# Optimization experiments

Hardware: AMD Instinct MI355X
Metric: run time of the kernel (lower is better)

Reference implementation:

```python
import jax, jax.numpy as jnp
import numpy as np

D_MODEL, N_QUERY, N_HEAD = 1024, 2, 8
D_HEAD = D_MODEL // (N_QUERY * N_HEAD)  # 64
KV = D_HEAD * N_HEAD                    # 512


def setup_inputs() -> dict:
    key = jax.random.key(0)
    ks = jax.random.split(key, 6)
    B, S = 2, 2048
    x = jax.random.normal(ks[0], (B, S, D_MODEL), jnp.float32)
    Wq = jax.random.normal(ks[1], (D_MODEL, D_MODEL), jnp.float32) / np.sqrt(D_MODEL)
    Wk = jax.random.normal(ks[2], (D_MODEL, KV), jnp.float32) / np.sqrt(D_MODEL)
    Wv = jax.random.normal(ks[3], (D_MODEL, KV), jnp.float32) / np.sqrt(D_MODEL)
    memory = jax.random.normal(ks[4], (KV, KV), jnp.float32)
    memory_norm = jnp.ones((KV,), jnp.float32)
    memory_weight = jnp.ones((1,), jnp.float32)
    return {"x": x, "Wq": Wq, "Wk": Wk, "Wv": Wv,
            "memory": memory, "memory_norm": memory_norm,
            "memory_weight": memory_weight}


def reference(x, Wq, Wk, Wv, memory, memory_norm, memory_weight):
    B, S, _ = x.shape
    QH = N_QUERY * N_HEAD
    scale = 1.0 / jnp.sqrt(jnp.float32(D_HEAD))

    q = x @ Wq          # (B,S,D_MODEL)
    k = x @ Wk          # (B,S,KV)
    v = x @ Wv          # (B,S,KV)

    # --- Eq. 6: grouped scaled dot-product attention ---
    q4 = q.reshape(B, S, QH, D_HEAD)                    # flat query split
    k4 = jnp.repeat(k.reshape(B, S, N_HEAD, D_HEAD), N_QUERY, axis=2)  # (B,S,QH,D)
    v4 = jnp.repeat(v.reshape(B, S, N_HEAD, D_HEAD), N_QUERY, axis=2)
    scores = jnp.einsum('bsnd,btnd->bnst', q4, k4) * scale  # (B,QH,S,S)
    probs = jax.nn.softmax(scores, axis=-1)
    a_dot = jnp.einsum('bnst,btnd->bsnd', probs, v4)        # (B,S,QH,D)

    # --- Eq. 7: memory read (grouped over n_query, width n_head*d_head) ---
    sigma_q = jax.nn.elu(q.reshape(B, S, N_QUERY, KV))      # (B,S,Q,KV)
    num = sigma_q @ memory                                   # (B,S,Q,KV)
    den = (sigma_q @ memory_norm)[..., None]                 # (B,S,Q,1)
    a_mem = (num / den).reshape(B, S, QH, D_HEAD)

    # --- Eq. 8/9: memory update (delta rule) ---
    sigma_k = jax.nn.elu(k)                                  # (B,S,KV)
    retrieved = (sigma_k @ memory) / (sigma_k @ memory_norm)[..., None]
    new_memory = memory + jnp.einsum('bsk,bsv->kv', sigma_k, v - retrieved)
    new_memory_norm = memory_norm + jnp.sum(sigma_k, axis=(0, 1))

    # --- Eq. 10: sigmoid-gated fusion ---
    w = jax.nn.sigmoid(memory_weight)                        # (1,)
    out = (a_dot * (1.0 - w) + a_mem * w).reshape(B, S, D_MODEL)
    return out, new_memory, new_memory_norm
```

## Files before the change

kernel.cpp:

```cpp
#include <hip/hip_runtime.h>
#include <hip/hip_bf16.h>

#define BB 2
#define SS 2048
#define DM 1024
#define KVD 512
#define NH 8
#define NQ 2
#define QH 16
#define DH 64
#define MROWS 4096

typedef float f32x4 __attribute__((ext_vector_type(4)));
typedef short short8 __attribute__((ext_vector_type(8)));
typedef short short4v __attribute__((ext_vector_type(4)));
typedef unsigned uint2v __attribute__((ext_vector_type(2)));

__device__ __forceinline__ float elu_f(float x) {
    return x > 0.0f ? x : (__expf(x) - 1.0f);
}

__device__ __forceinline__ short f2bf(float f) {
    union { float f; unsigned u; } v; v.f = f;
    unsigned r = v.u + 0x7FFFu + ((v.u >> 16) & 1u);
    return (short)(r >> 16);
}
__device__ __forceinline__ float bf2f(short s) {
    union { unsigned u; float f; } v;
    v.u = ((unsigned)(unsigned short)s) << 16;
    return v.f;
}
__device__ __forceinline__ unsigned cvtpk(float lo, float hi) {
    unsigned u;
    asm("v_cvt_pk_bf16_f32 %0, %1, %2" : "=v"(u) : "v"(lo), "v"(hi));
    return u;
}

__device__ __forceinline__ int swzs(int row, int byteoff) {
    return (row * 128 + (byteoff ^ ((row & 7) << 4))) >> 1;
}

#define GLD16(gp, lp) __builtin_amdgcn_global_load_lds( \
    (const __attribute__((address_space(1))) void*)(gp), \
    (__attribute__((address_space(3))) void*)(lp), 16, 0, 0)

__device__ __forceinline__ void stage_gl(const short* __restrict__ src, int ld,
                                         int row0, int k0, short* L,
                                         int wv, int lane) {
    const int srow = lane >> 3, sslot = lane & 7;
    #pragma unroll
    for (int i = 0; i < 4; i++) {
        int row = wv * 32 + i * 8 + srow;
        int slot = sslot ^ (row & 7);
        GLD16(&src[(size_t)(row0 + row) * ld + k0 + slot * 8],
              &L[(wv * 32 + i * 8) * 64]);
    }
}

__device__ __forceinline__ void mma_tile(const short* __restrict__ Als,
                                         const short* __restrict__ Bls,
                                         int mb, int nb, int qr, int kg,
                                         f32x4 acc[4][4]) {
    #pragma unroll
    for (int kc = 0; kc < 2; kc++) {
        short8 af[4], bg[4];
        #pragma unroll
        for (int mi = 0; mi < 4; mi++)
            af[mi] = *(const short8*)&Als[swzs(mb + mi * 16 + qr, kc * 64 + kg * 16)];
        #pragma unroll
        for (int ni = 0; ni < 4; ni++)
            bg[ni] = *(const short8*)&Bls[swzs(nb + ni * 16 + qr, kc * 64 + kg * 16)];
        #pragma unroll
        for (int mi = 0; mi < 4; mi++)
            #pragma unroll
            for (int ni = 0; ni < 4; ni++)
                acc[mi][ni] = __builtin_amdgcn_mfma_f32_16x16x32_bf16(
                    af[mi], bg[ni], acc[mi][ni], 0, 0, 0);
    }
}

__global__ __launch_bounds__(256) void convert_x(
        const float* __restrict__ x, short* __restrict__ xb) {
    int i = (blockIdx.x * 256 + threadIdx.x) * 8;
    float4 a = *(const float4*)&x[i];
    float4 b = *(const float4*)&x[i + 4];
    short8 s;
    s[0] = f2bf(a.x); s[1] = f2bf(a.y); s[2] = f2bf(a.z); s[3] = f2bf(a.w);
    s[4] = f2bf(b.x); s[5] = f2bf(b.y); s[6] = f2bf(b.z); s[7] = f2bf(b.w);
    *(short8*)&xb[i] = s;
}

__global__ __launch_bounds__(256) void transpose_w(
        const float* __restrict__ Wq, const float* __restrict__ Wk,
        const float* __restrict__ Wv, short* __restrict__ wtb) {
    __shared__ float Ts[64][65];
    const int k0 = blockIdx.x * 64, n0 = blockIdx.y * 64;
    const float* W; int ld, c0;
    if (n0 < 1024)      { W = Wq; ld = 1024; c0 = n0; }
    else if (n0 < 1536) { W = Wk; ld = 512;  c0 = n0 - 1024; }
    else                { W = Wv; ld = 512;  c0 = n0 - 1536; }
    const int tid = threadIdx.x;
    #pragma unroll
    for (int i = 0; i < 16; i++) {
        int e = tid + 256 * i;
        int kk = e >> 6, nn = e & 63;
        Ts[nn][kk] = W[(size_t)(k0 + kk) * ld + c0 + nn];
    }
    __syncthreads();
    #pragma unroll
    for (int i = 0; i < 16; i++) {
        int e = tid + 256 * i;
        int nn = e >> 6, kk = e & 63;
        wtb[(size_t)(n0 + nn) * 1024 + k0 + kk] = f2bf(Ts[nn][kk]);
    }
}

__global__ __launch_bounds__(256) void transpose_mem(
        const float* __restrict__ m, short* __restrict__ memtb) {
    __shared__ float Ts[64][65];
    const int k0 = blockIdx.x * 64, n0 = blockIdx.y * 64;
    const int tid = threadIdx.x;
    #pragma unroll
    for (int i = 0; i < 16; i++) {
        int e = tid + 256 * i;
        int kk = e >> 6, nn = e & 63;
        Ts[nn][kk] = m[(size_t)(k0 + kk) * 512 + n0 + nn];
    }
    __syncthreads();
    #pragma unroll
    for (int i = 0; i < 16; i++) {
        int e = tid + 256 * i;
        int nn = e >> 6, kk = e & 63;
        memtb[(size_t)(n0 + nn) * 512 + k0 + kk] = f2bf(Ts[nn][kk]);
    }
}

__global__ __launch_bounds__(256) void transpose_vT(
        const short* __restrict__ vbuf, short* __restrict__ vt) {
    __shared__ short Ts[64][65];
    const int s0 = blockIdx.x * 64;
    const int bh2 = blockIdx.y;
    const int b = bh2 >> 3, kvh = bh2 & 7;
    const int tid = threadIdx.x;
    #pragma unroll
    for (int i = 0; i < 16; i++) {
        int e = tid + 256 * i;
        int tl = e >> 6, d = e & 63;
        Ts[d][tl] = vbuf[(size_t)(b * SS + s0 + tl) * KVD + kvh * DH + d];
    }
    __syncthreads();
    #pragma unroll
    for (int i = 0; i < 16; i++) {
        int e = tid + 256 * i;
        int d = e >> 6, tc = e & 63;
        vt[((size_t)bh2 * DH + d) * SS + s0 + tc] = Ts[d][tc];
    }
}

__global__ __launch_bounds__(256) void elu_rows(
        const short* __restrict__ qb, const short* __restrict__ kbuf,
        const float* __restrict__ norm,
        short* __restrict__ qelu, short* __restrict__ kelu,
        float* __restrict__ den_q, float* __restrict__ den_k) {
    const int wavei = threadIdx.x >> 6, lane = threadIdx.x & 63;
    const int row = blockIdx.x * 4 + wavei;
    const short* src; short* dst; float* den;
    if (row < 8192) {
        src = qb + (size_t)row * 512; dst = qelu + (size_t)row * 512;
        den = den_q + row;
    } else {
        int rk = row - 8192;
        src = kbuf + (size_t)rk * 512; dst = kelu + (size_t)rk * 512;
        den = den_k + rk;
    }
    short8 v = *(const short8*)&src[lane * 8];
    float4 n0 = *(const float4*)&norm[lane * 8];
    float4 n1 = *(const float4*)&norm[lane * 8 + 4];
    float nn[8] = {n0.x, n0.y, n0.z, n0.w, n1.x, n1.y, n1.z, n1.w};
    float s = 0.0f;
    short8 o;
    #pragma unroll
    for (int j = 0; j < 8; j++) {
        float e = elu_f(bf2f(v[j]));
        o[j] = f2bf(e);
        s += e * nn[j];
    }
    *(short8*)&dst[lane * 8] = o;
    #pragma unroll
    for (int off = 32; off >= 1; off >>= 1) s += __shfl_xor(s, off);
    if (lane == 0) *den = s;
}

__global__ __launch_bounds__(256) void transpose_kelu(
        const short* __restrict__ kelu, short* __restrict__ keluT) {
    __shared__ short Ts[64][65];
    const int s0 = blockIdx.x * 64, i0 = blockIdx.y * 64;
    const int tid = threadIdx.x;
    #pragma unroll
    for (int i = 0; i < 16; i++) {
        int e = tid + 256 * i;
        int ss = e >> 6, ii = e & 63;
        Ts[ii][ss] = kelu[(size_t)(s0 + ss) * 512 + i0 + ii];
    }
    __syncthreads();
    #pragma unroll
    for (int i = 0; i < 16; i++) {
        int e = tid + 256 * i;
        int ii = e >> 6, ss = e & 63;
        keluT[(size_t)(i0 + ii) * 4096 + s0 + ss] = Ts[ii][ss];
    }
}

__global__ __launch_bounds__(256) void gemm_qkv_mfma(
        const short* __restrict__ xb, const short* __restrict__ wtb,
        short* __restrict__ q, short* __restrict__ k, short* __restrict__ v) {
    __shared__ __align__(16) short Als[8192];
    __shared__ __align__(16) short Bls[8192];
    const int n0 = blockIdx.x * 128, m0 = blockIdx.y * 128;
    const int tid = threadIdx.x, lane = tid & 63, wv = tid >> 6;
    const int qr = lane & 15, kg = lane >> 4;
    const int mb = (wv >> 1) * 64, nb = (wv & 1) * 64;

    f32x4 acc[4][4];
    #pragma unroll
    for (int i = 0; i < 4; i++)
        #pragma unroll
        for (int j = 0; j < 4; j++) acc[i][j] = (f32x4){0.f, 0.f, 0.f, 0.f};

    for (int kt = 0; kt < 16; kt++) {
        stage_gl(xb, 1024, m0, kt * 64, Als, wv, lane);
        stage_gl(wtb, 1024, n0, kt * 64, Bls, wv, lane);
        __syncthreads();
        mma_tile(Als, Bls, mb, nb, qr, kg, acc);
        __syncthreads();
    }

    short* dst; int ldo, c0;
    if (n0 < 1024)      { dst = q; ldo = 1024; c0 = n0; }
    else if (n0 < 1536) { dst = k; ldo = 512;  c0 = n0 - 1024; }
    else                { dst = v; ldo = 512;  c0 = n0 - 1536; }
    #pragma unroll
    for (int mi = 0; mi < 4; mi++)
        #pragma unroll
        for (int ni = 0; ni < 4; ni++)
            #pragma unroll
            for (int r = 0; r < 4; r++) {
                int gr = m0 + mb + mi * 16 + kg * 4 + r;
                int gc = c0 + nb + ni * 16 + qr;
                dst[(size_t)gr * ldo + gc] = f2bf(acc[mi][ni][r]);
            }
}

__global__ __launch_bounds__(256) void gemm_amem_mfma(
        const short* __restrict__ qelu, const short* __restrict__ memtb,
        const float* __restrict__ den_q, const float* __restrict__ mw,
        float* __restrict__ out) {
    __shared__ __align__(16) short Als[8192];
    __shared__ __align__(16) short Bls[8192];
    const int n0 = blockIdx.x * 128, m0 = blockIdx.y * 128;
    const int tid = threadIdx.x, lane = tid & 63, wv = tid >> 6;
    const int qr = lane & 15, kg = lane >> 4;
    const int mb = (wv >> 1) * 64, nb = (wv & 1) * 64;
    const float wgt = 1.0f / (1.0f + __expf(-mw[0]));

    f32x4 acc[4][4];
    #pragma unroll
    for (int i = 0; i < 4; i++)
        #pragma unroll
        for (int j = 0; j < 4; j++) acc[i][j] = (f32x4){0.f, 0.f, 0.f, 0.f};

    for (int kt = 0; kt < 8; kt++) {
        stage_gl(qelu, 512, m0, kt * 64, Als, wv, lane);
        stage_gl(memtb, 512, n0, kt * 64, Bls, wv, lane);
        __syncthreads();
        mma_tile(Als, Bls, mb, nb, qr, kg, acc);
        __syncthreads();
    }

    #pragma unroll
    for (int mi = 0; mi < 4; mi++) {
        int gr0 = m0 + mb + mi * 16 + kg * 4;
        float invd[4];
        #pragma unroll
        for (int r = 0; r < 4; r++) invd[r] = wgt / den_q[gr0 + r];
        #pragma unroll
        for (int ni = 0; ni < 4; ni++) {
            int gc = n0 + nb + ni * 16 + qr;
            #pragma unroll
            for (int r = 0; r < 4; r++) {
                size_t fo = (size_t)(gr0 + r) * 512 + gc;
                out[fo] = out[fo] + acc[mi][ni][r] * invd[r];
            }
        }
    }
}

__global__ __launch_bounds__(256) void gemm_u_mfma(
        const short* __restrict__ kelu, const short* __restrict__ memtb,
        const short* __restrict__ vb, const float* __restrict__ den_k,
        short* __restrict__ uT) {
    __shared__ __align__(16) short Als[8192];
    __shared__ __align__(16) short Bls[8192];
    const int n0 = blockIdx.x * 128, m0 = blockIdx.y * 128;
    const int tid = threadIdx.x, lane = tid & 63, wv = tid >> 6;
    const int qr = lane & 15, kg = lane >> 4;
    const int mb = (wv >> 1) * 64, nb = (wv & 1) * 64;

    f32x4 acc[4][4];
    #pragma unroll
    for (int i = 0; i < 4; i++)
        #pragma unroll
        for (int j = 0; j < 4; j++) acc[i][j] = (f32x4){0.f, 0.f, 0.f, 0.f};

    for (int kt = 0; kt < 8; kt++) {
        stage_gl(kelu, 512, m0, kt * 64, Als, wv, lane);
        stage_gl(memtb, 512, n0, kt * 64, Bls, wv, lane);
        __syncthreads();
        mma_tile(Als, Bls, mb, nb, qr, kg, acc);
        __syncthreads();
    }

    #pragma unroll
    for (int mi = 0; mi < 4; mi++) {
        int gr0 = m0 + mb + mi * 16 + kg * 4;
        float invd[4];
        #pragma unroll
        for (int r = 0; r < 4; r++) invd[r] = 1.0f / den_k[gr0 + r];
        #pragma unroll
        for (int ni = 0; ni < 4; ni++) {
            int gc = n0 + nb + ni * 16 + qr;
            short4v st;
            #pragma unroll
            for (int r = 0; r < 4; r++)
                st[r] = f2bf(bf2f(vb[(size_t)(gr0 + r) * 512 + gc])
                             - acc[mi][ni][r] * invd[r]);
            *(short4v*)&uT[(size_t)gc * 4096 + gr0] = st;
        }
    }
}

__global__ __launch_bounds__(256) void gemm_delta_mfma(
        const short* __restrict__ keluT, const short* __restrict__ uT,
        float* __restrict__ dpart) {
    __shared__ __align__(16) short Als[8192];
    __shared__ __align__(16) short Bls[8192];
    const int j0 = blockIdx.x * 128, i0 = blockIdx.y * 128;
    const int kcz = blockIdx.z;
    const int tid = threadIdx.x, lane = tid & 63, wv = tid >> 6;
    const int qr = lane & 15, kg = lane >> 4;
    const int mb = (wv >> 1) * 64, nb = (wv & 1) * 64;

    f32x4 acc[4][4];
    #pragma unroll
    for (int i = 0; i < 4; i++)
        #pragma unroll
        for (int j = 0; j < 4; j++) acc[i][j] = (f32x4){0.f, 0.f, 0.f, 0.f};

    for (int kt = 0; kt < 4; kt++) {
        int k0 = kcz * 256 + kt * 64;
        stage_gl(keluT, 4096, i0, k0, Als, wv, lane);
        stage_gl(uT, 4096, j0, k0, Bls, wv, lane);
        __syncthreads();
        mma_tile(Als, Bls, mb, nb, qr, kg, acc);
        __syncthreads();
    }

    #pragma unroll
    for (int mi = 0; mi < 4; mi++)
        #pragma unroll
        for (int ni = 0; ni < 4; ni++)
            #pragma unroll
            for (int r = 0; r < 4; r++) {
                int gr = i0 + mb + mi * 16 + kg * 4 + r;
                int gc = j0 + nb + ni * 16 + qr;
                dpart[(size_t)kcz * (KVD * KVD) + (size_t)gr * 512 + gc] = acc[mi][ni][r];
            }
}

__global__ __launch_bounds__(256) void delta_final(
        const float* __restrict__ part, const float* __restrict__ memory,
        float* __restrict__ out_mem) {
    const int idx = blockIdx.x * 256 + threadIdx.x;
    float s = memory[idx];
    #pragma unroll
    for (int kc = 0; kc < 16; kc++) s += part[(size_t)kc * (KVD * KVD) + idx];
    out_mem[idx] = s;
}

__global__ __launch_bounds__(256) void colsum_rows(
        const short* __restrict__ keluT, const float* __restrict__ mnorm,
        float* __restrict__ out_norm) {
    const int wavei = threadIdx.x >> 6, lane = threadIdx.x & 63;
    const int row = blockIdx.x * 4 + wavei;
    float s = 0.0f;
    #pragma unroll
    for (int j = 0; j < 8; j++) {
        short8 v = *(const short8*)&keluT[(size_t)row * 4096 + j * 512 + lane * 8];
        #pragma unroll
        for (int e = 0; e < 8; e++) s += bf2f(v[e]);
    }
    #pragma unroll
    for (int off = 32; off >= 1; off >>= 1) s += __shfl_xor(s, off);
    if (lane == 0) out_norm[row] = mnorm[row] + s;
}

__global__ __launch_bounds__(256) void flash_attn_mfma(
        const short* __restrict__ qb, const short* __restrict__ kb,
        const short* __restrict__ vt, const float* __restrict__ mw,
        float* __restrict__ out) {
    __shared__ __align__(16) short Klds[2][4096];
    __shared__ __align__(16) short Vlds[2][4096];
    __shared__ __align__(16) short Plds[4096];

    const int r0 = blockIdx.x * 64;
    const int bh = blockIdx.y;
    const int b = bh >> 4, qh = bh & 15;
    const int kvh = qh >> 1;
    const int tid = threadIdx.x;
    const int lane = tid & 63, wv = tid >> 6;
    const int qr = lane & 15, kg = lane >> 4;
    const float scale2 = 0.125f * 1.44269504f;
    const float wgt = 1.0f / (1.0f + __expf(-mw[0]));

    const int srow = lane >> 3, sslot = lane & 7;
    const short* kbase = kb + (size_t)(b * SS) * KVD + kvh * DH;
    const short* vbase = vt + (size_t)(b * NH + kvh) * DH * SS;

    short8 qa[2];
    {
        const short* qp = qb + (size_t)(b * SS + r0 + wv * 16 + qr) * DM + qh * DH;
        qa[0] = *(const short8*)&qp[kg * 8];
        qa[1] = *(const short8*)&qp[32 + kg * 8];
        #pragma unroll
        for (int e = 0; e < 8; e++) {
            qa[0][e] = f2bf(bf2f(qa[0][e]) * scale2);
            qa[1][e] = f2bf(bf2f(qa[1][e]) * scale2);
        }
    }
    short8 ones;
    #pragma unroll
    for (int e = 0; e < 8; e++) ones[e] = (short)0x3F80;

    f32x4 oacc[4];
    #pragma unroll
    for (int dt = 0; dt < 4; dt++) oacc[dt] = (f32x4){0.f, 0.f, 0.f, 0.f};
    f32x4 lacc = (f32x4){0.f, 0.f, 0.f, 0.f};
    float m_i = -1e30f;

    short* Pw = Plds + wv * 1024;

    auto stage = [&](int t0, int bf) {
        #pragma unroll
        for (int i = 0; i < 2; i++) {
            int row = wv * 16 + i * 8 + srow;
            int slot = sslot ^ (row & 7);
            GLD16(&kbase[(size_t)(t0 + row) * KVD + slot * 8],
                  &Klds[bf][(wv * 16 + i * 8) * 64]);
            GLD16(&vbase[(size_t)row * SS + t0 + slot * 8],
                  &Vlds[bf][(wv * 16 + i * 8) * 64]);
        }
    };

    stage(0, 0);

    for (int it = 0; it < 32; ++it) {
        const int cur = it & 1;
        __syncthreads();
        if (it + 1 < 32) stage((it + 1) * 64, cur ^ 1);

        f32x4 sacc[4];
        #pragma unroll
        for (int j = 0; j < 4; j++) sacc[j] = (f32x4){0.f, 0.f, 0.f, 0.f};
        __builtin_amdgcn_s_setprio(1);
        #pragma unroll
        for (int c = 0; c < 2; c++) {
            #pragma unroll
            for (int j = 0; j < 4; j++) {
                short8 kf = *(const short8*)&Klds[cur][swzs(j * 16 + qr, kg * 16 + c * 64)];
                sacc[j] = __builtin_amdgcn_mfma_f32_16x16x32_bf16(kf, qa[c], sacc[j], 0, 0, 0);
            }
        }
        __builtin_amdgcn_s_setprio(0);

        float m0a = fmaxf(fmaxf(sacc[0][0], sacc[0][1]), fmaxf(sacc[0][2], sacc[0][3]));
        float m0b = fmaxf(fmaxf(sacc[1][0], sacc[1][1]), fmaxf(sacc[1][2], sacc[1][3]));
        float m0c = fmaxf(fmaxf(sacc[2][0], sacc[2][1]), fmaxf(sacc[2][2], sacc[2][3]));
        float m0d = fmaxf(fmaxf(sacc[3][0], sacc[3][1]), fmaxf(sacc[3][2], sacc[3][3]));
        float rm = fmaxf(fmaxf(m0a, m0b), fmaxf(m0c, m0d));
        rm = fmaxf(rm, __shfl_xor(rm, 16));
        rm = fmaxf(rm, __shfl_xor(rm, 32));
        if (rm > m_i + 8.0f) {
            float resc = exp2f(m_i - rm);
            m_i = rm;
            lacc *= resc;
            #pragma unroll
            for (int dt = 0; dt < 4; dt++) oacc[dt] *= resc;
        }
        #pragma unroll
        for (int j = 0; j < 4; j++) {
            float p0 = exp2f(sacc[j][0] - m_i);
            float p1 = exp2f(sacc[j][1] - m_i);
            float p2 = exp2f(sacc[j][2] - m_i);
            float p3 = exp2f(sacc[j][3] - m_i);
            uint2v u;
            u[0] = cvtpk(p0, p1);
            u[1] = cvtpk(p2, p3);
            *(uint2v*)&Pw[swzs(qr, j * 32 + kg * 8)] = u;
        }
        asm volatile("s_waitcnt lgkmcnt(0)" ::: "memory");
        __builtin_amdgcn_sched_barrier(0);

        __builtin_amdgcn_s_setprio(1);
        #pragma unroll
        for (int c = 0; c < 2; c++) {
            short8 pf = *(const short8*)&Pw[swzs(qr, kg * 16 + c * 64)];
            lacc = __builtin_amdgcn_mfma_f32_16x16x32_bf16(ones, pf, lacc, 0, 0, 0);
            #pragma unroll
            for (int dt = 0; dt < 4; dt++) {
                short8 vf = *(const short8*)&Vlds[cur][swzs(dt * 16 + qr, kg * 16 + c * 64)];
                oacc[dt] = __builtin_amdgcn_mfma_f32_16x16x32_bf16(vf, pf, oacc[dt], 0, 0, 0);
            }
        }
        __builtin_amdgcn_s_setprio(0);
    }

    float inv = (1.0f - wgt) / lacc[0];
    float* outp = out + (size_t)(b * SS + r0 + wv * 16 + qr) * DM + qh * DH;
    #pragma unroll
    for (int dt = 0; dt < 4; dt++) {
        f32x4 st;
        #pragma unroll
        for (int r = 0; r < 4; r++) st[r] = oacc[dt][r] * inv;
        *(f32x4*)&outp[dt * 16 + kg * 4] = st;
    }
}

extern "C" void kernel_launch(void* const* d_in, const int* in_sizes, int n_in,
                              void* d_out, int out_size, void* d_ws, size_t ws_size,
                              hipStream_t stream) {
    const float* x      = (const float*)d_in[0];
    const float* Wq     = (const float*)d_in[1];
    const float* Wk     = (const float*)d_in[2];
    const float* Wv     = (const float*)d_in[3];
    const float* memory = (const float*)d_in[4];
    const float* mnorm  = (const float*)d_in[5];
    const float* mw     = (const float*)d_in[6];

    float* out_f   = (float*)d_out;
    float* out_mem = out_f + (size_t)MROWS * DM;
    float* out_nrm = out_mem + (size_t)KVD * KVD;

    short*  xb    = (short*)d_ws;
    short*  wtb   = xb + 4194304;
    short*  memtb = wtb + 2097152;
    short*  qb    = memtb + 262144;
    short*  kbuf  = qb + 4194304;
    short*  vbuf  = kbuf + 2097152;
    short*  vt    = vbuf + 2097152;
    short*  qelu  = vt + 2097152;
    short*  kelu  = qelu + 4194304;
    short*  keluT = kelu + 2097152;
    short*  uT    = keluT + 2097152;
    float*  den_q = (float*)(uT + 2097152);
    float*  den_k = den_q + 8192;
    float*  dpart = (float*)d_ws;

    convert_x<<<2048, 256, 0, stream>>>(x, xb);
    transpose_w<<<dim3(16, 32), 256, 0, stream>>>(Wq, Wk, Wv, wtb);
    transpose_mem<<<dim3(8, 8), 256, 0, stream>>>(memory, memtb);

    gemm_qkv_mfma<<<dim3(16, 32), 256, 0, stream>>>(xb, wtb, qb, kbuf, vbuf);
    transpose_vT<<<dim3(32, 16), 256, 0, stream>>>(vbuf, vt);
    elu_rows<<<3072, 256, 0, stream>>>(qb, kbuf, mnorm, qelu, kelu, den_q, den_k);

    flash_attn_mfma<<<dim3(32, 32), 256, 0, stream>>>(qb, kbuf, vt, mw, out_f);

    gemm_amem_mfma<<<dim3(4, 64), 256, 0, stream>>>(qelu, memtb, den_q, mw, out_f);

    transpose_kelu<<<dim3(64, 8), 256, 0, stream>>>(kelu, keluT);
    colsum_rows<<<128, 256, 0, stream>>>(keluT, mnorm, out_nrm);

    gemm_u_mfma<<<dim3(4, 32), 256, 0, stream>>>(kelu, memtb, vbuf, den_k, uT);
    gemm_delta_mfma<<<dim3(4, 4, 16), 256, 0, stream>>>(keluT, uT, dpart);
    delta_final<<<1024, 256, 0, stream>>>(dpart, memory, out_mem);
}
```

Baseline: 178.8 us.

## Fuse prep kernels, fold ELU and transposes into QKV GEMM epilogue

Merges the x conversion and the weight and memory transposes into one prep launch. The QKV GEMM epilogue now also writes the ELU of q and k, the transposed k-ELU and the transposed V directly, so the separate transpose and ELU kernels go away. The denominator and column-sum reductions are merged into one kernel. This cuts launch count and intermediate round trips, but the epilogue now does strided, uncoalesced scattered stores for keluT and vt, and the denominators are computed from bf16-rounded ELU values instead of fp32.

New measurement: 177.3 us. No clear change (-0.8%).

```diff
diff --git a/kernel.cpp b/kernel.cpp
--- a/kernel.cpp
+++ b/kernel.cpp
@@ -79,141 +79,72 @@
     }
 }
 
-__global__ __launch_bounds__(256) void convert_x(
-        const float* __restrict__ x, short* __restrict__ xb) {
-    int i = (blockIdx.x * 256 + threadIdx.x) * 8;
-    float4 a = *(const float4*)&x[i];
-    float4 b = *(const float4*)&x[i + 4];
-    short8 s;
-    s[0] = f2bf(a.x); s[1] = f2bf(a.y); s[2] = f2bf(a.z); s[3] = f2bf(a.w);
-    s[4] = f2bf(b.x); s[5] = f2bf(b.y); s[6] = f2bf(b.z); s[7] = f2bf(b.w);
-    *(short8*)&xb[i] = s;
-}
-
-__global__ __launch_bounds__(256) void transpose_w(
-        const float* __restrict__ Wq, const float* __restrict__ Wk,
-        const float* __restrict__ Wv, short* __restrict__ wtb) {
+__global__ __launch_bounds__(256) void prep_all(
+        const float* __restrict__ x, const float* __restrict__ Wq,
+        const float* __restrict__ Wk, const float* __restrict__ Wv,
+        const float* __restrict__ memory,
+        short* __restrict__ xb, short* __restrict__ wtb,
+        short* __restrict__ memtb) {
     __shared__ float Ts[64][65];
-    const int k0 = blockIdx.x * 64, n0 = blockIdx.y * 64;
-    const float* W; int ld, c0;
-    if (n0 < 1024)      { W = Wq; ld = 1024; c0 = n0; }
-    else if (n0 < 1536) { W = Wk; ld = 512;  c0 = n0 - 1024; }
-    else                { W = Wv; ld = 512;  c0 = n0 - 1536; }
+    const int blk = blockIdx.x;
     const int tid = threadIdx.x;
-    #pragma unroll
-    for (int i = 0; i < 16; i++) {
-        int e = tid + 256 * i;
-        int kk = e >> 6, nn = e & 63;
-        Ts[nn][kk] = W[(size_t)(k0 + kk) * ld + c0 + nn];
-    }
-    __syncthreads();
-    #pragma unroll
-    for (int i = 0; i < 16; i++) {
-        int e = tid + 256 * i;
-        int nn = e >> 6, kk = e & 63;
-        wtb[(size_t)(n0 + nn) * 1024 + k0 + kk] = f2bf(Ts[nn][kk]);
-    }
-}
-
-__global__ __launch_bounds__(256) void transpose_mem(
-        const float* __restrict__ m, short* __restrict__ memtb) {
-    __shared__ float Ts[64][65];
-    const int k0 = blockIdx.x * 64, n0 = blockIdx.y * 64;
-    const int tid = threadIdx.x;
-    #pragma unroll
-    for (int i = 0; i < 16; i++) {
-        int e = tid + 256 * i;
-        int kk = e >> 6, nn = e & 63;
-        Ts[nn][kk] = m[(size_t)(k0 + kk) * 512 + n0 + nn];
-    }
-    __syncthreads();
-    #pragma unroll
-    for (int i = 0; i < 16; i++) {
-        int e = tid + 256 * i;
-        int nn = e >> 6, kk = e & 63;
-        memtb[(size_t)(n0 + nn) * 512 + k0 + kk] = f2bf(Ts[nn][kk]);
-    }
-}
-
-__global__ __launch_bounds__(256) void transpose_vT(
-        const short* __restrict__ vbuf, short* __restrict__ vt) {
-    __shared__ short Ts[64][65];
-    const int s0 = blockIdx.x * 64;
-    const int bh2 = blockIdx.y;
-    const int b = bh2 >> 3, kvh = bh2 & 7;
-    const int tid = threadIdx.x;
-    #pragma unroll
-    for (int i = 0; i < 16; i++) {
-        int e = tid + 256 * i;
-        int tl = e >> 6, d = e & 63;
-        Ts[d][tl] = vbuf[(size_t)(b * SS + s0 + tl) * KVD + kvh * DH + d];
-    }
-    __syncthreads();
-    #pragma unroll
-    for (int i = 0; i < 16; i++) {
-        int e = tid + 256 * i;
-        int d = e >> 6, tc = e & 63;
-        vt[((size_t)bh2 * DH + d) * SS + s0 + tc] = Ts[d][tc];
-    }
-}
-
-__global__ __launch_bounds__(256) void elu_rows(
-        const short* __restrict__ qb, const short* __restrict__ kbuf,
-        const float* __restrict__ norm,
-        short* __restrict__ qelu, short* __restrict__ kelu,
-        float* __restrict__ den_q, float* __restrict__ den_k) {
-    const int wavei = threadIdx.x >> 6, lane = threadIdx.x & 63;
-    const int row = blockIdx.x * 4 + wavei;
-    const short* src; short* dst; float* den;
-    if (row < 8192) {
-        src = qb + (size_t)row * 512; dst = qelu + (size_t)row * 512;
-        den = den_q + row;
-    } else {
-        int rk = row - 8192;
-        src = kbuf + (size_t)rk * 512; dst = kelu + (size_t)rk * 512;
-        den = den_k + rk;
-    }
-    short8 v = *(const short8*)&src[lane * 8];
-    float4 n0 = *(const float4*)&norm[lane * 8];
-    float4 n1 = *(const float4*)&norm[lane * 8 + 4];
-    float nn[8] = {n0.x, n0.y, n0.z, n0.w, n1.x, n1.y, n1.z, n1.w};
-    float s = 0.0f;
-    short8 o;
-    #pragma unroll
-    for (int j = 0; j < 8; j++) {
-        float e = elu_f(bf2f(v[j]));
-        o[j] = f2bf(e);
-        s += e * nn[j];
-    }
-    *(short8*)&dst[lane * 8] = o;
-    #pragma unroll
-    for (int off = 32; off >= 1; off >>= 1) s += __shfl_xor(s, off);
-    if (lane == 0) *den = s;
-}
-
-__global__ __launch_bounds__(256) void transpose_kelu(
-        const short* __restrict__ kelu, short* __restrict__ keluT) {
-    __shared__ short Ts[64][65];
-    const int s0 = blockIdx.x * 64, i0 = blockIdx.y * 64;
-    const int tid = threadIdx.x;
-    #pragma unroll
-    for (int i = 0; i < 16; i++) {
-        int e = tid + 256 * i;
-        int ss = e >> 6, ii = e & 63;
-        Ts[ii][ss] = kelu[(size_t)(s0 + ss) * 512 + i0 + ii];
-    }
-    __syncthreads();
-    #pragma unroll
-    for (int i = 0; i < 16; i++) {
-        int e = tid + 256 * i;
-        int ii = e >> 6, ss = e & 63;
-        keluT[(size_t)(i0 + ii) * 4096 + s0 + ss] = Ts[ii][ss];
+
+    if (blk < 2048) {
+        int i = (blk * 256 + tid) * 8;
+        float4 a = *(const float4*)&x[i];
+        float4 b = *(const float4*)&x[i + 4];
+        short8 s;
+        s[0] = f2bf(a.x); s[1] = f2bf(a.y); s[2] = f2bf(a.z); s[3] = f2bf(a.w);
+        s[4] = f2bf(b.x); s[5] = f2bf(b.y); s[6] = f2bf(b.z); s[7] = f2bf(b.w);
+        *(short8*)&xb[i] = s;
+        return;
+    }
+    if (blk < 2560) {
+        int idx = blk - 2048;
+        const int k0 = (idx & 15) * 64, n0 = (idx >> 4) * 64;
+        const float* W; int ld, c0;
+        if (n0 < 1024)      { W = Wq; ld = 1024; c0 = n0; }
+        else if (n0 < 1536) { W = Wk; ld = 512;  c0 = n0 - 1024; }
+        else                { W = Wv; ld = 512;  c0 = n0 - 1536; }
+        #pragma unroll
+        for (int i = 0; i < 16; i++) {
+            int e = tid + 256 * i;
+            int kk = e >> 6, nn = e & 63;
+            Ts[nn][kk] = W[(size_t)(k0 + kk) * ld + c0 + nn];
+        }
+        __syncthreads();
+        #pragma unroll
+        for (int i = 0; i < 16; i++) {
+            int e = tid + 256 * i;
+            int nn = e >> 6, kk = e & 63;
+            wtb[(size_t)(n0 + nn) * 1024 + k0 + kk] = f2bf(Ts[nn][kk]);
+        }
+        return;
+    }
+    {
+        int idx = blk - 2560;
+        const int k0 = (idx & 7) * 64, n0 = (idx >> 3) * 64;
+        #pragma unroll
+        for (int i = 0; i < 16; i++) {
+            int e = tid + 256 * i;
+            int kk = e >> 6, nn = e & 63;
+            Ts[nn][kk] = memory[(size_t)(k0 + kk) * 512 + n0 + nn];
+        }
+        __syncthreads();
+        #pragma unroll
+        for (int i = 0; i < 16; i++) {
+            int e = tid + 256 * i;
+            int nn = e >> 6, kk = e & 63;
+            memtb[(size_t)(n0 + nn) * 512 + k0 + kk] = f2bf(Ts[nn][kk]);
+        }
     }
 }
 
 __global__ __launch_bounds__(256) void gemm_qkv_mfma(
         const short* __restrict__ xb, const short* __restrict__ wtb,
-        short* __restrict__ q, short* __restrict__ k, short* __restrict__ v) {
+        short* __restrict__ q, short* __restrict__ k, short* __restrict__ v,
+        short* __restrict__ qelu, short* __restrict__ kelu,
+        short* __restrict__ keluT, short* __restrict__ vt) {
     __shared__ __align__(16) short Als[8192];
     __shared__ __align__(16) short Bls[8192];
     const int n0 = blockIdx.x * 128, m0 = blockIdx.y * 128;
@@ -235,10 +166,7 @@
         __syncthreads();
     }
 
-    short* dst; int ldo, c0;
-    if (n0 < 1024)      { dst = q; ldo = 1024; c0 = n0; }
-    else if (n0 < 1536) { dst = k; ldo = 512;  c0 = n0 - 1024; }
-    else                { dst = v; ldo = 512;  c0 = n0 - 1536; }
+    const int kind = (n0 < 1024) ? 0 : (n0 < 1536) ? 1 : 2;
     #pragma unroll
     for (int mi = 0; mi < 4; mi++)
         #pragma unroll
@@ -246,9 +174,62 @@
             #pragma unroll
             for (int r = 0; r < 4; r++) {
                 int gr = m0 + mb + mi * 16 + kg * 4 + r;
-                int gc = c0 + nb + ni * 16 + qr;
-                dst[(size_t)gr * ldo + gc] = f2bf(acc[mi][ni][r]);
+                short val = f2bf(acc[mi][ni][r]);
+                if (kind == 0) {
+                    int gc = n0 + nb + ni * 16 + qr;
+                    q[(size_t)gr * 1024 + gc] = val;
+                    qelu[(size_t)(gr * 2 + (gc >> 9)) * 512 + (gc & 511)]
+                        = f2bf(elu_f(bf2f(val)));
+                } else if (kind == 1) {
+                    int gc = (n0 - 1024) + nb + ni * 16 + qr;
+                    k[(size_t)gr * 512 + gc] = val;
+                    short ev = f2bf(elu_f(bf2f(val)));
+                    kelu[(size_t)gr * 512 + gc] = ev;
+                    keluT[(size_t)gc * 4096 + gr] = ev;
+                } else {
+                    int gc = (n0 - 1536) + nb + ni * 16 + qr;
+                    v[(size_t)gr * 512 + gc] = val;
+                    vt[(((size_t)(gr >> 11) * 8 + (gc >> 6)) * 64 + (gc & 63)) * SS
+                       + (gr & 2047)] = val;
+                }
             }
+}
+
+__global__ __launch_bounds__(256) void den_colsum(
+        const short* __restrict__ qelu, const short* __restrict__ kelu,
+        const short* __restrict__ keluT, const float* __restrict__ norm,
+        float* __restrict__ den_q, float* __restrict__ den_k,
+        float* __restrict__ out_norm) {
+    const int wavei = threadIdx.x >> 6, lane = threadIdx.x & 63;
+    const int blk = blockIdx.x;
+    if (blk < 3072) {
+        const int row = blk * 4 + wavei;
+        const short* src; float* den;
+        if (row < 8192) { src = qelu + (size_t)row * 512; den = den_q + row; }
+        else { int rk = row - 8192; src = kelu + (size_t)rk * 512; den = den_k + rk; }
+        short8 vv = *(const short8*)&src[lane * 8];
+        float4 n0 = *(const float4*)&norm[lane * 8];
+        float4 n1 = *(const float4*)&norm[lane * 8 + 4];
+        float nn[8] = {n0.x, n0.y, n0.z, n0.w, n1.x, n1.y, n1.z, n1.w};
+        float s = 0.0f;
+        #pragma unroll
+        for (int j = 0; j < 8; j++) s += bf2f(vv[j]) * nn[j];
+        #pragma unroll
+        for (int off = 32; off >= 1; off >>= 1) s += __shfl_xor(s, off);
+        if (lane == 0) *den = s;
+    } else {
+        const int row = (blk - 3072) * 4 + wavei;
+        float s = 0.0f;
+        #pragma unroll
+        for (int j = 0; j < 8; j++) {
+            short8 vv = *(const short8*)&keluT[(size_t)row * 4096 + j * 512 + lane * 8];
+            #pragma unroll
+            for (int e = 0; e < 8; e++) s += bf2f(vv[e]);
+        }
+        #pragma unroll
+        for (int off = 32; off >= 1; off >>= 1) s += __shfl_xor(s, off);
+        if (lane == 0) out_norm[row] = norm[row] + s;
+    }
 }
 
 __global__ __launch_bounds__(256) void gemm_amem_mfma(
@@ -385,23 +366,6 @@
     #pragma unroll
     for (int kc = 0; kc < 16; kc++) s += part[(size_t)kc * (KVD * KVD) + idx];
     out_mem[idx] = s;
-}
-
-__global__ __launch_bounds__(256) void colsum_rows(
-        const short* __restrict__ keluT, const float* __restrict__ mnorm,
-        float* __restrict__ out_norm) {
-    const int wavei = threadIdx.x >> 6, lane = threadIdx.x & 63;
-    const int row = blockIdx.x * 4 + wavei;
-    float s = 0.0f;
-    #pragma unroll
-    for (int j = 0; j < 8; j++) {
-        short8 v = *(const short8*)&keluT[(size_t)row * 4096 + j * 512 + lane * 8];
-        #pragma unroll
-        for (int e = 0; e < 8; e++) s += bf2f(v[e]);
-    }
-    #pragma unroll
-    for (int off = 32; off >= 1; off >>= 1) s += __shfl_xor(s, off);
-    if (lane == 0) out_norm[row] = mnorm[row] + s;
 }
 
 __global__ __launch_bounds__(256) void flash_attn_mfma(
@@ -565,20 +529,17 @@
     float*  den_k = den_q + 8192;
     float*  dpart = (float*)d_ws;
 
-    convert_x<<<2048, 256, 0, stream>>>(x, xb);
-    transpose_w<<<dim3(16, 32), 256, 0, stream>>>(Wq, Wk, Wv, wtb);
-    transpose_mem<<<dim3(8, 8), 256, 0, stream>>>(memory, memtb);
-
-    gemm_qkv_mfma<<<dim3(16, 32), 256, 0, stream>>>(xb, wtb, qb, kbuf, vbuf);
-    transpose_vT<<<dim3(32, 16), 256, 0, stream>>>(vbuf, vt);
-    elu_rows<<<3072, 256, 0, stream>>>(qb, kbuf, mnorm, qelu, kelu, den_q, den_k);
+    prep_all<<<2624, 256, 0, stream>>>(x, Wq, Wk, Wv, memory, xb, wtb, memtb);
+
+    gemm_qkv_mfma<<<dim3(16, 32), 256, 0, stream>>>(xb, wtb, qb, kbuf, vbuf,
+                                                    qelu, kelu, keluT, vt);
 
     flash_attn_mfma<<<dim3(32, 32), 256, 0, stream>>>(qb, kbuf, vt, mw, out_f);
 
+    den_colsum<<<3200, 256, 0, stream>>>(qelu, kelu, keluT, mnorm,
+                                         den_q, den_k, out_nrm);
+
     gemm_amem_mfma<<<dim3(4, 64), 256, 0, stream>>>(qelu, memtb, den_q, mw, out_f);
-
-    transpose_kelu<<<dim3(64, 8), 256, 0, stream>>>(kelu, keluT);
-    colsum_rows<<<128, 256, 0, stream>>>(keluT, mnorm, out_nrm);
 
     gemm_u_mfma<<<dim3(4, 32), 256, 0, stream>>>(kelu, memtb, vbuf, den_k, uT);
     gemm_delta_mfma<<<dim3(4, 4, 16), 256, 0, stream>>>(keluT, uT, dpart);
```
